# Performance work log

Measured on AMD Instinct MI355X. Metric: run time of the kernel, lower is better.

The kernel has to match this reference:

```python
import jax, jax.numpy as jnp
import numpy as np

HIDDEN = 1024
HEADS = 8
HEAD = HIDDEN // HEADS
EPS = 1e-5


def _gammas():
    lo = np.log(1.0 / 512.0)
    hi = np.log(1.0 / 32.0)
    lin = np.linspace(lo, hi, HEADS)
    return jnp.asarray(1.0 - np.exp(lin), dtype=jnp.float32)  # [H]


def setup_inputs() -> dict:
    key = jax.random.key(0)
    ks = jax.random.split(key, 7)
    B, S = 2, 2048
    x = jax.random.normal(ks[0], (B, S, HIDDEN), dtype=jnp.float32)
    # Per-head retention projection weights (Retention(head_size, gamma)): [H, d, d]
    Wq = jax.random.normal(ks[1], (HEADS, HEAD, HEAD), dtype=jnp.float32) / HEAD
    Wk = jax.random.normal(ks[2], (HEADS, HEAD, HEAD), dtype=jnp.float32) / HEAD
    Wv = jax.random.normal(ks[3], (HEADS, HEAD, HEAD), dtype=jnp.float32) / HEAD
    W1 = jax.random.normal(ks[4], (HIDDEN, HIDDEN), dtype=jnp.float32) / HIDDEN
    W2 = jax.random.normal(ks[5], (HIDDEN, HIDDEN), dtype=jnp.float32) / HIDDEN
    gn_w = jnp.ones((HIDDEN,), dtype=jnp.float32)
    gn_b = jnp.zeros((HIDDEN,), dtype=jnp.float32)
    return {"x": x, "Wq": Wq, "Wk": Wk, "Wv": Wv, "W1": W1, "W2": W2,
            "gn_w": gn_w, "gn_b": gn_b}


def _decay_mask(S, gammas):
    idx = jnp.arange(S)
    diff = idx[:, None] - idx[None, :]              # [S, S]
    causal = diff >= 0
    safe = jnp.where(causal, diff, 0).astype(jnp.float32)
    D = jnp.where(causal[None], gammas[:, None, None] ** safe[None], 0.0)  # [H,S,S]
    return D


def _msr_forward(x, Wq, Wk, Wv, W1, W2, gn_w, gn_b):
    B, S, _ = x.shape
    xh = x.reshape(B, S, HEADS, HEAD)               # per-head slices
    q = jnp.einsum('bshd,hde->bshe', xh, Wq)
    k = jnp.einsum('bshd,hde->bshe', xh, Wk)
    v = jnp.einsum('bshd,hde->bshe', xh, Wv)
    D = _decay_mask(S, _gammas())                   # [H,S,S]
    scores = jnp.einsum('bnhd,bmhd->bhnm', q, k) * D[None]
    ret = jnp.einsum('bhnm,bmhd->bnhd', scores, v)  # [B,S,H,d]
    # GroupNorm(num_groups=H, channels=HIDDEN) over flattened rows
    mu = jnp.mean(ret, axis=-1, keepdims=True)
    var = jnp.var(ret, axis=-1, keepdims=True)
    ret = (ret - mu) * jax.lax.rsqrt(var + EPS)
    ret = ret.reshape(B, S, HIDDEN) * gn_w + gn_b
    gated = x @ W1
    out = gated * jax.nn.sigmoid(gated) + ret       # swish gate + residual add
    return out @ W2


def reference(x, Wq, Wk, Wv, W1, W2, gn_w, gn_b):
    return _msr_forward(x, Wq, Wk, Wv, W1, W2, gn_w, gn_b)
```

## Files before the change

### kernel.cpp

```cpp
#include <hip/hip_runtime.h>
#include <hip/hip_bf16.h>

#define HID 1024
#define NH 8
#define HD 128
#define BB 2
#define SS 2048
#define CHK 128
#define NCH 16

typedef __attribute__((ext_vector_type(8))) short short8;
typedef __attribute__((ext_vector_type(4))) float f32x4;

static __device__ __forceinline__ float b2f(unsigned short u){
  unsigned int x = ((unsigned int)u) << 16; float f;
  __builtin_memcpy(&f, &x, 4); return f;
}
static __device__ __forceinline__ unsigned short f2b(float f){
  unsigned int x; __builtin_memcpy(&x, &f, 4);
  x += 0x7fffu + ((x >> 16) & 1u);
  return (unsigned short)(x >> 16);
}
static __device__ __forceinline__ float head_gamma(int h){
  double lo = -6.238324625039508;
  double hi = -3.4657359027997265;
  double lin = lo + (hi - lo) * ((double)h / 7.0);
  return (float)(1.0 - exp(lin));
}
static __device__ __forceinline__ f32x4 MFMA(short8 a, short8 b, f32x4 c){
  return __builtin_amdgcn_mfma_f32_16x16x32_bf16(a, b, c, 0, 0, 0);
}

typedef const __attribute__((address_space(1))) unsigned int* gas1_u32p;
typedef __attribute__((address_space(3))) unsigned int* las3_u32p;
static __device__ __forceinline__ void gload_lds16(const void* g, void* l){
  __builtin_amdgcn_global_load_lds((gas1_u32p)g, (las3_u32p)l, 16, 0, 0);
}

__global__ __launch_bounds__(256) void k_prep(
    const float* __restrict__ W1, unsigned short* __restrict__ w1T,
    const float* __restrict__ W2, unsigned short* __restrict__ w2T,
    const float* __restrict__ Wq, unsigned short* __restrict__ wqT,
    const float* __restrict__ Wk, unsigned short* __restrict__ wkT,
    const float* __restrict__ Wv, unsigned short* __restrict__ wvT)
{
  int bid = blockIdx.x, t = threadIdx.x;
  __shared__ float tile[32][33];
  const float* in; unsigned short* out; int R, C, r0, c0;
  if (bid < 2048){
    int which = bid >> 10;
    int local = bid & 1023;
    in  = which ? W2 : W1;  out = which ? w2T : w1T;
    R = C = HID;
    c0 = (local & 31)*32; r0 = (local >> 5)*32;
  } else {
    int local = bid - 2048;
    int mat = local >> 7;
    int rem = local & 127;
    int z = rem >> 4, tl2 = rem & 15;
    const float* ws[3] = { Wq, Wk, Wv };
    unsigned short* os[3] = { wqT, wkT, wvT };
    in  = ws[mat] + (size_t)z*HD*HD;
    out = os[mat] + (size_t)z*HD*HD;
    R = C = HD;
    c0 = (tl2 & 3)*32; r0 = (tl2 >> 2)*32;
  }
  int tx = t & 31, ty = t >> 5;
  #pragma unroll
  for (int i=0;i<4;i++) tile[ty+i*8][tx] = in[(size_t)(r0+ty+i*8)*C + c0+tx];
  __syncthreads();
  #pragma unroll
  for (int i=0;i<4;i++) out[(size_t)(c0+ty+i*8)*R + r0+tx] = f2b(tile[tx][ty+i*8]);
}

__global__ __launch_bounds__(256) void k_qkv(
    const float* __restrict__ x,
    const unsigned short* __restrict__ wqT,
    const unsigned short* __restrict__ wkT,
    const unsigned short* __restrict__ wvT,
    unsigned short* __restrict__ xb,
    unsigned short* __restrict__ qb,
    unsigned short* __restrict__ kb,
    unsigned short* __restrict__ ktsb,
    unsigned short* __restrict__ vtb)
{
  int bid = blockIdx.x;
  int stile = bid & 31;
  int bh = bid >> 5;
  int h = bh & 7, b = bh >> 3;
  int T0 = stile*64;
  int chunk = stile >> 1, pm0 = (stile & 1)*64;
  float l2g = log2f(head_gamma(h));
  __shared__ unsigned short tl[128*72];
  int t = threadIdx.x, wv = t>>6, l = t&63, lr = l&15, lg = l>>4;
  int row0 = T0 + wv*16;
  short8 a[4];
  const float* xp = x + (size_t)(b*SS + row0 + lr)*HID + h*HD + lg*8;
  unsigned short* xbw = xb + (size_t)(b*SS + row0 + lr)*HID + h*HD + lg*8;
  #pragma unroll
  for (int kk=0;kk<4;kk++){
    float4 v0 = *(const float4*)(xp + kk*32);
    float4 v1 = *(const float4*)(xp + kk*32 + 4);
    unsigned short tmp[8] = { f2b(v0.x), f2b(v0.y), f2b(v0.z), f2b(v0.w),
                              f2b(v1.x), f2b(v1.y), f2b(v1.z), f2b(v1.w) };
    a[kk] = *(const short8*)tmp;
    *(short8*)(xbw + kk*32) = a[kk];
  }
  size_t obase = ((size_t)bh*SS + row0)*HD;
  size_t tbase = ((size_t)(bh*NCH + chunk))*HD*CHK + pm0;

  auto wout = [&](unsigned short* dst){
    int e = t & 127, th = t >> 7;
    const uint4* src = (const uint4*)(tl + e*72 + th*32);
    uint4* d4 = (uint4*)(dst + (size_t)e*CHK + th*32);
    #pragma unroll
    for (int i=0;i<4;i++) d4[i] = src[i];
  };

  {
    const unsigned short* wb = wqT + (size_t)h*HD*HD;
    unsigned short* op = qb + obase;
    #pragma unroll
    for (int nt=0;nt<8;nt++){
      f32x4 acc = {0.f,0.f,0.f,0.f};
      #pragma unroll
      for (int kk=0;kk<4;kk++){
        short8 bfr = *(const short8*)(wb + (size_t)(nt*16+lr)*HD + kk*32 + lg*8);
        acc = MFMA(a[kk], bfr, acc);
      }
      #pragma unroll
      for (int r=0;r<4;r++)
        op[(size_t)(lg*4+r)*HD + nt*16 + lr] = f2b(acc[r]);
    }
  }
  {
    const unsigned short* wb = wkT + (size_t)h*HD*HD;
    unsigned short* op = kb + obase;
    float ksc[4];
    #pragma unroll
    for (int r=0;r<4;r++)
      ksc[r] = exp2f((float)(127 - (pm0 + wv*16 + lg*4 + r))*l2g);
    #pragma unroll
    for (int nt=0;nt<8;nt++){
      f32x4 acc = {0.f,0.f,0.f,0.f};
      #pragma unroll
      for (int kk=0;kk<4;kk++){
        short8 bfr = *(const short8*)(wb + (size_t)(nt*16+lr)*HD + kk*32 + lg*8);
        acc = MFMA(a[kk], bfr, acc);
      }
      #pragma unroll
      for (int r=0;r<4;r++){
        op[(size_t)(lg*4+r)*HD + nt*16 + lr] = f2b(acc[r]);
        tl[(nt*16+lr)*72 + wv*16 + lg*4 + r] = f2b(acc[r]*ksc[r]);
      }
    }
  }
  __syncthreads();
  wout(ktsb + tbase);
  __syncthreads();
  {
    const unsigned short* wb = wvT + (size_t)h*HD*HD;
    #pragma unroll
    for (int nt=0;nt<8;nt++){
      f32x4 acc = {0.f,0.f,0.f,0.f};
      #pragma unroll
      for (int kk=0;kk<4;kk++){
        short8 bfr = *(const short8*)(wb + (size_t)(nt*16+lr)*HD + kk*32 + lg*8);
        acc = MFMA(a[kk], bfr, acc);
      }
      #pragma unroll
      for (int r=0;r<4;r++)
        tl[(nt*16+lr)*72 + wv*16 + lg*4 + r] = f2b(acc[r]);
    }
  }
  __syncthreads();
  wout(vtb + tbase);
}

__global__ __launch_bounds__(256) void k_sumscan(
    const unsigned short* __restrict__ ktsb,
    const unsigned short* __restrict__ vtb,
    unsigned short* __restrict__ ST)
{
  int bid = blockIdx.x;
  int dh = bid & 1, et = (bid >> 1) & 7, bh = bid >> 4;
  int h = bh & 7;
  float d128 = exp2f(128.f * log2f(head_gamma(h)));
  int t = threadIdx.x, wv = t>>6, l = t&63, lr = l&15, lg = l>>4;
  int e0 = et*16;
  int d0w = dh*64 + wv*16;
  const unsigned short* vt = vtb  + (size_t)bh*NCH*HD*CHK;
  const unsigned short* kt = ktsb + (size_t)bh*NCH*HD*CHK;
  unsigned short* Sb = ST + (size_t)bh*NCH*HD*HD;

  f32x4 s = {0.f,0.f,0.f,0.f};
  #pragma unroll
  for (int c=0;c<NCH;c++){
    const unsigned short* vc = vt + (size_t)c*HD*CHK;
    const unsigned short* kc = kt + (size_t)c*HD*CHK;
    f32x4 acc = {0.f,0.f,0.f,0.f};
    #pragma unroll
    for (int kk=0;kk<4;kk++){
      short8 af = *(const short8*)(vc + (size_t)(e0+lr)*CHK + kk*32 + lg*8);
      short8 bf = *(const short8*)(kc + (size_t)(d0w+lr)*CHK + kk*32 + lg*8);
      acc = MFMA(af, bf, acc);
    }
    unsigned short* So = Sb + (size_t)c*HD*HD;
    #pragma unroll
    for (int r=0;r<4;r++){
      So[(size_t)(e0+lg*4+r)*HD + d0w + lr] = f2b(s[r]);
      s[r] = s[r]*d128 + acc[r];
    }
  }
}

__global__ __launch_bounds__(512) void k_g1ret(
    const unsigned short* __restrict__ A,
    const unsigned short* __restrict__ BT,
    const unsigned short* __restrict__ qb,
    const unsigned short* __restrict__ kb,
    const unsigned short* __restrict__ vtb,
    const unsigned short* __restrict__ ST,
    const float* __restrict__ gnw,
    const float* __restrict__ gnb,
    unsigned short* __restrict__ Cb,
    int M, int N, int K)
{
  __shared__ unsigned short lsu[65536];
  const int nb = N >> 7;
  const int nwg = (M >> 7) * nb;
  const int cpx = nwg >> 3;
  int bid0 = blockIdx.x;
  int bid = (bid0 & 7)*cpx + (bid0 >> 3);
  const int m0 = (bid / nb) << 7;
  const int n0 = (bid % nb) << 7;
  const int t = threadIdx.x, wv = t>>6, l = t&63, lr = l&15, lg = l>>4;
  const int wr = (wv>>1)<<5;
  const int wc = (wv&1)<<6;
  const int srow = l >> 3;
  const int sgc  = ((l & 7) ^ srow) << 3;
  const unsigned short* Abase = A  + (size_t)(m0 + wv*16 + srow)*K + sgc;
  const unsigned short* Bbase = BT + (size_t)(n0 + wv*16 + srow)*K + sgc;

  auto stage = [&](int buf, int kt){
    unsigned short* la = lsu + buf*16384;
    unsigned short* lb = la + 8192;
    int k0 = kt << 6;
    #pragma unroll
    for (int it=0; it<2; ++it){
      gload_lds16(Abase + (size_t)(it*8)*K + k0, la + (wv*16 + it*8)*64);
      gload_lds16(Bbase + (size_t)(it*8)*K + k0, lb + (wv*16 + it*8)*64);
    }
  };
  auto stageMat = [&](const unsigned short* g, int reg){
    #pragma unroll
    for (int i=0;i<4;i++){
      int c = i*512 + t;
      int row = c >> 4, p = c & 15;
      gload_lds16(g + row*128 + ((p ^ (row & 7)) << 3),
                  lsu + reg + (i*512 + (t & 448))*8);
    }
  };

  const int b = m0 >> 11, j = (m0 >> 7) & 15, h = n0 >> 7;
  const int bh = b*NH + h;
  const int cj = bh*NCH + j;
  float l2g = log2f(head_gamma(h));
  const unsigned short* qc = qb + ((size_t)bh*SS + j*CHK)*HD;
  const unsigned short* kc = kb + ((size_t)bh*SS + j*CHK)*HD;
  const unsigned short* vt = vtb + (size_t)cj*HD*CHK;
  const unsigned short* Sp = ST + (size_t)cj*HD*HD;

  short8 qf[4];
  #pragma unroll
  for (int kk=0;kk<4;kk++)
    qf[kk] = *(const short8*)(qc + (size_t)(wv*16 + lr)*HD + kk*32 + lg*8);

  f32x4 acc[2][4];
  #pragma unroll
  for (int i=0;i<2;i++)
    #pragma unroll
    for (int j2=0;j2<4;j2++) acc[i][j2] = (f32x4){0,0,0,0};

  const int NT = K >> 6;
  stage(0,0); stage(1,1); stage(2,2);
  for (int kt = 0; kt < NT; ++kt){
    if (kt < NT-2)       asm volatile("s_waitcnt vmcnt(8)" ::: "memory");
    else if (kt == NT-2) asm volatile("s_waitcnt vmcnt(4)" ::: "memory");
    else                 asm volatile("s_waitcnt vmcnt(0)" ::: "memory");
    __builtin_amdgcn_s_barrier();
    __builtin_amdgcn_sched_barrier(0);
    if (kt+3 < NT) stage((kt+3)&3, kt+3);
    if (kt == NT-3) stageMat(Sp, 0);
    if (kt == NT-2) stageMat(vt, 16384);
    if (kt == NT-1) stageMat(kc, 32768);
    const unsigned short* pa = lsu + (kt&3)*16384;
    const unsigned short* pb = pa + 8192;
    #pragma unroll
    for (int ks=0; ks<2; ++ks){
      short8 af[2], bf[4];
      #pragma unroll
      for (int i=0;i<2;i++){
        int ra = wr + i*16 + lr;
        af[i] = *(const short8*)(pa + ra*64 + ((((ks<<2)+lg) ^ (ra&7))<<3));
      }
      #pragma unroll
      for (int j2=0;j2<4;j2++){
        int rb = wc + j2*16 + lr;
        bf[j2] = *(const short8*)(pb + rb*64 + ((((ks<<2)+lg) ^ (rb&7))<<3));
      }
      #pragma unroll
      for (int i=0;i<2;i++)
        #pragma unroll
        for (int j2=0;j2<4;j2++)
          acc[i][j2] = MFMA(af[i], bf[j2], acc[i][j2]);
    }
  }
  __syncthreads();

  f32x4 racc[8];
  #pragma unroll
  for (int nt=0;nt<8;nt++){
    f32x4 aa = {0,0,0,0};
    #pragma unroll
    for (int kk=0;kk<4;kk++){
      short8 bfr = *(const short8*)(lsu + (nt*16+lr)*128 + (((kk*4+lg) ^ (lr&7))<<3));
      aa = MFMA(qf[kk], bfr, aa);
    }
    racc[nt] = aa;
  }
  #pragma unroll
  for (int r=0;r<4;r++){
    int n = wv*16 + lg*4 + r;
    float sf = exp2f((float)(n+1)*l2g);
    #pragma unroll
    for (int nt=0;nt<8;nt++) racc[nt][r] *= sf;
  }
  __syncthreads();

  int ntmax = (wv | 1) + 1;
  for (int nt=0; nt<ntmax; nt++){
    f32x4 a0 = {0,0,0,0};
    #pragma unroll
    for (int kk=0;kk<4;kk++){
      short8 bfr = *(const short8*)(lsu + 32768 + (nt*16+lr)*128 + (((kk*4+lg) ^ (lr&7))<<3));
      a0 = MFMA(qf[kk], bfr, a0);
    }
    int col = nt*16 + lr;
    #pragma unroll
    for (int r=0;r<4;r++){
      int lrow = wv*16 + lg*4 + r;
      float v0 = (col <= lrow) ? a0[r]*exp2f((float)(lrow-col)*l2g) : 0.f;
      lsu[lrow*128 + (((col>>3) ^ (lrow&7))<<3) + (col&7)] = f2b(v0);
    }
  }

  #pragma unroll
  for (int i=0;i<2;i++){
    #pragma unroll
    for (int j2=0;j2<4;j2++){
      #pragma unroll
      for (int r=0;r<4;r++){
        int row = wr + i*16 + lg*4 + r;
        int col = wc + j2*16 + lr;
        float v = acc[i][j2][r];
        lsu[49152 + row*128 + (((col>>3) ^ (row&7))<<3) + (col&7)]
          = f2b(v / (1.f + __expf(-v)));
      }
    }
  }

  int ksmax = (wv >> 1) + 1;
  for (int ks=0; ks<ksmax; ks++){
    short8 afr = *(const short8*)(lsu + (wv*16+lr)*128 + (((ks*4+lg) ^ (lr&7))<<3));
    #pragma unroll
    for (int nt=0;nt<8;nt++){
      short8 bfr = *(const short8*)(lsu + 16384 + (nt*16+lr)*128 + (((ks*4+lg) ^ (lr&7))<<3));
      racc[nt] = MFMA(afr, bfr, racc[nt]);
    }
  }
  __syncthreads();

  const float* gw  = gnw + h*HD;
  const float* gbb = gnb + h*HD;
  #pragma unroll
  for (int r=0;r<4;r++){
    float s = 0.f, ss = 0.f;
    #pragma unroll
    for (int nt=0;nt<8;nt++){ float x2 = racc[nt][r]; s += x2; ss += x2*x2; }
    #pragma unroll
    for (int off=1; off<16; off<<=1){
      s  += __shfl_xor(s,  off, 64);
      ss += __shfl_xor(ss, off, 64);
    }
    float mu  = s*(1.f/128.f);
    float var = ss*(1.f/128.f) - mu*mu;
    float rs  = rsqrtf(var + 1e-5f);
    int Rr = wv*16 + lg*4 + r;
    #pragma unroll
    for (int nt=0;nt<8;nt++){
      int col = nt*16 + lr;
      float rv = (racc[nt][r]-mu)*rs*gw[col] + gbb[col];
      float cv = b2f(lsu[49152 + Rr*128 + (((col>>3) ^ (Rr&7))<<3) + (col&7)]);
      lsu[Rr*128 + (((col>>3) ^ (Rr&7))<<3) + (col&7)] = f2b(rv + cv);
    }
  }
  __syncthreads();

  {
    int row = t >> 2, cg = t & 3;
    unsigned short* orow = Cb + (size_t)(m0 + row)*N + n0 + cg*32;
    const unsigned short* lrp = lsu + row*128;
    #pragma unroll
    for (int i=0;i<4;i++){
      int c0 = cg*32 + i*8;
      *(uint4*)(orow + i*8) = *(const uint4*)(lrp + (((c0>>3) ^ (row&7))<<3));
    }
  }
}

__global__ __launch_bounds__(512) void k_gemm2(
    const unsigned short* __restrict__ A,
    const unsigned short* __restrict__ BT,
    float* __restrict__ Cf,
    int M, int N, int K)
{
  __shared__ unsigned short ls[4][2][128*64];
  const int nb = N >> 7;
  const int nwg = (M >> 7) * nb;
  const int cpx = nwg >> 3;
  int bid0 = blockIdx.x;
  int bid = (bid0 & 7)*cpx + (bid0 >> 3);
  const int m0 = (bid / nb) << 7;
  const int n0 = (bid % nb) << 7;
  const int t = threadIdx.x, wv = t>>6, l = t&63, lr = l&15, lg = l>>4;
  const int wr = (wv>>1)<<5;
  const int wc = (wv&1)<<6;
  const int srow = l >> 3;
  const int sgc  = ((l & 7) ^ srow) << 3;
  const unsigned short* Abase = A  + (size_t)(m0 + wv*16 + srow)*K + sgc;
  const unsigned short* Bbase = BT + (size_t)(n0 + wv*16 + srow)*K + sgc;

  auto stage = [&](int buf, int kt){
    unsigned short* la = &ls[buf][0][0];
    unsigned short* lb = &ls[buf][1][0];
    int k0 = kt << 6;
    #pragma unroll
    for (int it=0; it<2; ++it){
      gload_lds16(Abase + (size_t)(it*8)*K + k0, la + (wv*16 + it*8)*64);
      gload_lds16(Bbase + (size_t)(it*8)*K + k0, lb + (wv*16 + it*8)*64);
    }
  };

  f32x4 acc[2][4];
  #pragma unroll
  for (int i=0;i<2;i++)
    #pragma unroll
    for (int j=0;j<4;j++) acc[i][j] = (f32x4){0,0,0,0};

  const int NT = K >> 6;
  stage(0,0); stage(1,1); stage(2,2);
  for (int kt = 0; kt < NT; ++kt){
    if (kt < NT-2)       asm volatile("s_waitcnt vmcnt(8)" ::: "memory");
    else if (kt == NT-2) asm volatile("s_waitcnt vmcnt(4)" ::: "memory");
    else                 asm volatile("s_waitcnt vmcnt(0)" ::: "memory");
    __builtin_amdgcn_s_barrier();
    __builtin_amdgcn_sched_barrier(0);
    if (kt+3 < NT) stage((kt+3)&3, kt+3);
    const unsigned short* pa = &ls[kt&3][0][0];
    const unsigned short* pb = &ls[kt&3][1][0];
    #pragma unroll
    for (int ks=0; ks<2; ++ks){
      short8 af[2], bf[4];
      #pragma unroll
      for (int i=0;i<2;i++){
        int ra = wr + i*16 + lr;
        af[i] = *(const short8*)(pa + ra*64 + ((((ks<<2)+lg) ^ (ra&7))<<3));
      }
      #pragma unroll
      for (int j=0;j<4;j++){
        int rb = wc + j*16 + lr;
        bf[j] = *(const short8*)(pb + rb*64 + ((((ks<<2)+lg) ^ (rb&7))<<3));
      }
      #pragma unroll
      for (int i=0;i<2;i++)
        #pragma unroll
        for (int j=0;j<4;j++)
          acc[i][j] = MFMA(af[i], bf[j], acc[i][j]);
    }
  }

  #pragma unroll
  for (int i=0;i<2;i++)
    #pragma unroll
    for (int j=0;j<4;j++)
      #pragma unroll
      for (int r=0;r<4;r++){
        int row = m0 + wr + i*16 + lg*4 + r;
        int col = n0 + wc + j*16 + lr;
        Cf[(size_t)row*N + col] = acc[i][j][r];
      }
}

extern "C" void kernel_launch(void* const* d_in, const int* in_sizes, int n_in,
                              void* d_out, int out_size, void* d_ws, size_t ws_size,
                              hipStream_t stream)
{
  (void)in_sizes; (void)n_in; (void)out_size; (void)ws_size;
  const float* x   = (const float*)d_in[0];
  const float* Wq  = (const float*)d_in[1];
  const float* Wk  = (const float*)d_in[2];
  const float* Wv  = (const float*)d_in[3];
  const float* W1  = (const float*)d_in[4];
  const float* W2  = (const float*)d_in[5];
  const float* gnw = (const float*)d_in[6];
  const float* gnb = (const float*)d_in[7];
  float* out = (float*)d_out;

  char* wsp = (char*)d_ws;
  size_t off = 0;
  auto alloc = [&](size_t bytes)->void*{
    off = (off + 255) & ~(size_t)255;
    void* p = wsp + off; off += bytes; return p;
  };
  const size_t NTOK = (size_t)BB*SS;
  unsigned short* xb   = (unsigned short*)alloc(NTOK*HID*2);
  unsigned short* w1T  = (unsigned short*)alloc((size_t)HID*HID*2);
  unsigned short* w2T  = (unsigned short*)alloc((size_t)HID*HID*2);
  unsigned short* wqT  = (unsigned short*)alloc((size_t)NH*HD*HD*2);
  unsigned short* wkT  = (unsigned short*)alloc((size_t)NH*HD*HD*2);
  unsigned short* wvT  = (unsigned short*)alloc((size_t)NH*HD*HD*2);
  unsigned short* qb   = (unsigned short*)alloc(NTOK*HID*2);
  unsigned short* kb   = (unsigned short*)alloc(NTOK*HID*2);
  unsigned short* ktsb = (unsigned short*)alloc(NTOK*HID*2);
  unsigned short* vtb  = (unsigned short*)alloc(NTOK*HID*2);
  unsigned short* ST   = (unsigned short*)alloc((size_t)BB*NH*NCH*HD*HD*2);
  unsigned short* opb  = (unsigned short*)alloc(NTOK*HID*2);

  k_prep<<<dim3(2432), dim3(256), 0, stream>>>(W1, w1T, W2, w2T,
                                               Wq, wqT, Wk, wkT, Wv, wvT);
  k_qkv<<<dim3(BB*NH*32), dim3(256), 0, stream>>>(x, wqT, wkT, wvT, xb, qb, kb, ktsb, vtb);
  k_sumscan<<<dim3(BB*NH*16), dim3(256), 0, stream>>>(ktsb, vtb, ST);

  k_g1ret<<<dim3(256), dim3(512), 0, stream>>>(xb, w1T, qb, kb, vtb, ST, gnw, gnb,
                                               opb, (int)NTOK, HID, HID);
  k_gemm2<<<dim3(256), dim3(512), 0, stream>>>(opb, w2T, out, (int)NTOK, HID, HID);
}
```

Before: 101.1 us.

## Move W1/W2 transpose into sumscan launch and store g1ret output directly

The W1/W2 fp32-to-bf16 transposes move out of the first prep kernel and are appended as extra blocks to the sumscan launch. The small QKV weight prep then finishes sooner, and the large transpose work fills idle CUs next to the 256-block sumscan. Separately, the retention+gate kernel's epilogue writes bf16 results straight to global memory instead of staging through LDS. This drops one barrier and the LDS round trip, at the cost of narrow 2-byte strided stores instead of 16-byte coalesced ones.

```diff
diff --git a/kernel.cpp b/kernel.cpp
--- a/kernel.cpp
+++ b/kernel.cpp
@@ -37,40 +37,27 @@
   __builtin_amdgcn_global_load_lds((gas1_u32p)g, (las3_u32p)l, 16, 0, 0);
 }
 
-__global__ __launch_bounds__(256) void k_prep(
-    const float* __restrict__ W1, unsigned short* __restrict__ w1T,
-    const float* __restrict__ W2, unsigned short* __restrict__ w2T,
+__global__ __launch_bounds__(256) void k_wqkv(
     const float* __restrict__ Wq, unsigned short* __restrict__ wqT,
     const float* __restrict__ Wk, unsigned short* __restrict__ wkT,
     const float* __restrict__ Wv, unsigned short* __restrict__ wvT)
 {
   int bid = blockIdx.x, t = threadIdx.x;
   __shared__ float tile[32][33];
-  const float* in; unsigned short* out; int R, C, r0, c0;
-  if (bid < 2048){
-    int which = bid >> 10;
-    int local = bid & 1023;
-    in  = which ? W2 : W1;  out = which ? w2T : w1T;
-    R = C = HID;
-    c0 = (local & 31)*32; r0 = (local >> 5)*32;
-  } else {
-    int local = bid - 2048;
-    int mat = local >> 7;
-    int rem = local & 127;
-    int z = rem >> 4, tl2 = rem & 15;
-    const float* ws[3] = { Wq, Wk, Wv };
-    unsigned short* os[3] = { wqT, wkT, wvT };
-    in  = ws[mat] + (size_t)z*HD*HD;
-    out = os[mat] + (size_t)z*HD*HD;
-    R = C = HD;
-    c0 = (tl2 & 3)*32; r0 = (tl2 >> 2)*32;
-  }
+  int mat = bid >> 7;
+  int rem = bid & 127;
+  int z = rem >> 4, tl2 = rem & 15;
+  const float* ws[3] = { Wq, Wk, Wv };
+  unsigned short* os[3] = { wqT, wkT, wvT };
+  const float* in = ws[mat] + (size_t)z*HD*HD;
+  unsigned short* out = os[mat] + (size_t)z*HD*HD;
+  int c0 = (tl2 & 3)*32, r0 = (tl2 >> 2)*32;
   int tx = t & 31, ty = t >> 5;
   #pragma unroll
-  for (int i=0;i<4;i++) tile[ty+i*8][tx] = in[(size_t)(r0+ty+i*8)*C + c0+tx];
-  __syncthreads();
-  #pragma unroll
-  for (int i=0;i<4;i++) out[(size_t)(c0+ty+i*8)*R + r0+tx] = f2b(tile[tx][ty+i*8]);
+  for (int i=0;i<4;i++) tile[ty+i*8][tx] = in[(size_t)(r0+ty+i*8)*HD + c0+tx];
+  __syncthreads();
+  #pragma unroll
+  for (int i=0;i<4;i++) out[(size_t)(c0+ty+i*8)*HD + r0+tx] = f2b(tile[tx][ty+i*8]);
 }
 
 __global__ __launch_bounds__(256) void k_qkv(
@@ -177,16 +164,34 @@
   wout(vtb + tbase);
 }
 
-__global__ __launch_bounds__(256) void k_sumscan(
+__global__ __launch_bounds__(256) void k_sumscanW(
     const unsigned short* __restrict__ ktsb,
     const unsigned short* __restrict__ vtb,
-    unsigned short* __restrict__ ST)
+    unsigned short* __restrict__ ST,
+    const float* __restrict__ W1, unsigned short* __restrict__ w1T,
+    const float* __restrict__ W2, unsigned short* __restrict__ w2T)
 {
-  int bid = blockIdx.x;
+  __shared__ float tile[32][33];
+  int bid = blockIdx.x, t = threadIdx.x;
+  if (bid >= 256){
+    int local = bid - 256;
+    int which = local >> 10;
+    int inner = local & 1023;
+    const float* in = which ? W2 : W1;
+    unsigned short* out = which ? w2T : w1T;
+    int c0 = (inner & 31)*32, r0 = (inner >> 5)*32;
+    int tx = t & 31, ty = t >> 5;
+    #pragma unroll
+    for (int i=0;i<4;i++) tile[ty+i*8][tx] = in[(size_t)(r0+ty+i*8)*HID + c0+tx];
+    __syncthreads();
+    #pragma unroll
+    for (int i=0;i<4;i++) out[(size_t)(c0+ty+i*8)*HID + r0+tx] = f2b(tile[tx][ty+i*8]);
+    return;
+  }
   int dh = bid & 1, et = (bid >> 1) & 7, bh = bid >> 4;
   int h = bh & 7;
   float d128 = exp2f(128.f * log2f(head_gamma(h)));
-  int t = threadIdx.x, wv = t>>6, l = t&63, lr = l&15, lg = l>>4;
+  int wv = t>>6, l = t&63, lr = l&15, lg = l>>4;
   int e0 = et*16;
   int d0w = dh*64 + wv*16;
   const unsigned short* vt = vtb  + (size_t)bh*NCH*HD*CHK;
@@ -381,6 +386,7 @@
   }
   __syncthreads();
 
+  unsigned short* op = Cb + (size_t)(m0 + wv*16)*N + n0;
   const float* gw  = gnw + h*HD;
   const float* gbb = gnb + h*HD;
   #pragma unroll
@@ -396,25 +402,15 @@
     float mu  = s*(1.f/128.f);
     float var = ss*(1.f/128.f) - mu*mu;
     float rs  = rsqrtf(var + 1e-5f);
-    int Rr = wv*16 + lg*4 + r;
+    int lrow = lg*4 + r;
+    int Rr = wv*16 + lrow;
+    unsigned short* orow = op + (size_t)lrow*N;
     #pragma unroll
     for (int nt=0;nt<8;nt++){
       int col = nt*16 + lr;
       float rv = (racc[nt][r]-mu)*rs*gw[col] + gbb[col];
       float cv = b2f(lsu[49152 + Rr*128 + (((col>>3) ^ (Rr&7))<<3) + (col&7)]);
-      lsu[Rr*128 + (((col>>3) ^ (Rr&7))<<3) + (col&7)] = f2b(rv + cv);
-    }
-  }
-  __syncthreads();
-
-  {
-    int row = t >> 2, cg = t & 3;
-    unsigned short* orow = Cb + (size_t)(m0 + row)*N + n0 + cg*32;
-    const unsigned short* lrp = lsu + row*128;
-    #pragma unroll
-    for (int i=0;i<4;i++){
-      int c0 = cg*32 + i*8;
-      *(uint4*)(orow + i*8) = *(const uint4*)(lrp + (((c0>>3) ^ (row&7))<<3));
+      orow[col] = f2b(rv + cv);
     }
   }
 }
@@ -537,11 +533,10 @@
   unsigned short* ST   = (unsigned short*)alloc((size_t)BB*NH*NCH*HD*HD*2);
   unsigned short* opb  = (unsigned short*)alloc(NTOK*HID*2);
 
-  k_prep<<<dim3(2432), dim3(256), 0, stream>>>(W1, w1T, W2, w2T,
-                                               Wq, wqT, Wk, wkT, Wv, wvT);
+  k_wqkv<<<dim3(384), dim3(256), 0, stream>>>(Wq, wqT, Wk, wkT, Wv, wvT);
   k_qkv<<<dim3(BB*NH*32), dim3(256), 0, stream>>>(x, wqT, wkT, wvT, xb, qb, kb, ktsb, vtb);
-  k_sumscan<<<dim3(BB*NH*16), dim3(256), 0, stream>>>(ktsb, vtb, ST);
-
+  k_sumscanW<<<dim3(BB*NH*16 + 2048), dim3(256), 0, stream>>>(ktsb, vtb, ST,
+                                                              W1, w1T, W2, w2T);
   k_g1ret<<<dim3(256), dim3(512), 0, stream>>>(xb, w1T, qb, kb, vtb, ST, gnw, gnb,
                                                opb, (int)NTOK, HID, HID);
   k_gemm2<<<dim3(256), dim3(512), 0, stream>>>(opb, w2T, out, (int)NTOK, HID, HID);
```

After: 98.08 us (median of 2 runs). 1.03x faster.
